# Kernel tuning notes

Measured on AMD Instinct MI355X. Metric: run time of the kernel, lower is better.

Reference implementation:

```python
import jax, jax.numpy as jnp
import numpy as np

IN_F = 1024
OUT_F = 1024
B, S = 8, 4096


def _pack_ternary(tern):
    # encoding: -1 -> 0, 0 -> 1, +1 -> 2; 4 values per byte, matching torch pack_ternary_weights
    enc = (tern + 1.0).astype(jnp.int32).reshape(-1)  # length divisible by 4 here
    return (enc[0::4] | (enc[1::4] << 2) | (enc[2::4] << 4) | (enc[3::4] << 6)).astype(jnp.int32)


def setup_inputs() -> dict:
    key = jax.random.key(0)
    kx, kw = jax.random.split(key)
    x = jax.random.normal(kx, (B, S, IN_F), dtype=jnp.float32)
    w = jax.random.normal(kw, (OUT_F, IN_F), dtype=jnp.float32) * 0.02
    # quantize_weights_158bit
    scale = jnp.maximum(jnp.mean(jnp.abs(w)), 1e-5)
    wn = w / scale
    tern = jnp.sign(wn) * (jnp.abs(wn) > 0.5).astype(jnp.float32)
    packed = _pack_ternary(tern)
    bias = jnp.zeros((OUT_F,), dtype=jnp.float32)
    return {"x": x, "packed_weight": packed, "weight_scale": scale.reshape(1), "bias": bias}


def reference(x, packed_weight, weight_scale, bias):
    n = OUT_F * IN_F
    shifts = jnp.array([0, 2, 4, 6], dtype=jnp.int32)
    # Faithful to original unpack_ternary_weights: concatenate bit-planes, then truncate.
    # (This is a permutation of the packed order, replicated deliberately.)
    enc = ((packed_weight[None, :] >> shifts[:, None]) & 3).reshape(-1)[:n]
    w = (enc.astype(jnp.float32) - 1.0).reshape(OUT_F, IN_F) * weight_scale  # dequant ternary
    # training path: INT8 per-token activation fake-quant
    act_scale = 127.0 / jnp.maximum(jnp.max(jnp.abs(x), axis=-1, keepdims=True), 1e-5)
    x_dq = jnp.clip(jnp.round(x * act_scale), -128.0, 127.0) / act_scale
    return jnp.einsum('bsi,oi->bso', x_dq, w) + bias
```

## Files before the change

### kernel.cpp

```cpp
#include <hip/hip_runtime.h>
#include <hip/hip_bf16.h>
#include <stdint.h>

typedef int i32x4 __attribute__((ext_vector_type(4)));

constexpr int IN_F = 1024;
constexpr int OUT_F = 1024;
constexpr int M_TOT = 8 * 4096;
constexpr int K_TOT = IN_F;
constexpr int N_TOT = OUT_F;

__global__ __launch_bounds__(256) void quant_kernel(
    const float* __restrict__ x,
    const float* __restrict__ wscale,
    int8_t* __restrict__ q,
    float* __restrict__ inv_row)
{
    const int row = blockIdx.x;
    const int t = threadIdx.x;
    const float4 v = reinterpret_cast<const float4*>(x + (size_t)row * IN_F)[t];
    float m = fmaxf(fmaxf(fabsf(v.x), fabsf(v.y)), fmaxf(fabsf(v.z), fabsf(v.w)));
    #pragma unroll
    for (int off = 32; off > 0; off >>= 1)
        m = fmaxf(m, __shfl_xor(m, off));
    __shared__ float smax[4];
    if ((t & 63) == 0) smax[t >> 6] = m;
    __syncthreads();
    m = fmaxf(fmaxf(smax[0], smax[1]), fmaxf(smax[2], smax[3]));
    const float a = fmaxf(m, 1e-5f);
    const float as = 127.0f / a;

    char4 o;
    o.x = (char)(int)fminf(fmaxf(rintf(v.x * as), -128.0f), 127.0f);
    o.y = (char)(int)fminf(fmaxf(rintf(v.y * as), -128.0f), 127.0f);
    o.z = (char)(int)fminf(fmaxf(rintf(v.z * as), -128.0f), 127.0f);
    o.w = (char)(int)fminf(fmaxf(rintf(v.w * as), -128.0f), 127.0f);
    reinterpret_cast<char4*>(q + (size_t)row * IN_F)[t] = o;
    if (t == 0) inv_row[row] = (a / 127.0f) * wscale[0];
}

__global__ __launch_bounds__(256) void unpack_kernel(
    const int* __restrict__ packed,
    int8_t* __restrict__ wt)
{
    const int o = blockIdx.x;
    const int k0 = threadIdx.x * 4;
    const int sh = (o >> 8) * 2;
    const int pbase = ((o & 255) << 10) + k0;
    const int4 pw = *reinterpret_cast<const int4*>(packed + pbase);
    char4 r;
    r.x = (char)(((pw.x >> sh) & 3) - 1);
    r.y = (char)(((pw.y >> sh) & 3) - 1);
    r.z = (char)(((pw.z >> sh) & 3) - 1);
    r.w = (char)(((pw.w >> sh) & 3) - 1);
    *reinterpret_cast<char4*>(wt + (size_t)o * IN_F + k0) = r;
}

constexpr int BM = 256, BN = 256, BK = 128;
constexpr int NT = K_TOT / BK;

__global__ __launch_bounds__(512, 2) void gemm_kernel(
    const int8_t* __restrict__ qa,
    const int8_t* __restrict__ wb,
    const float* __restrict__ inv_row,
    const float* __restrict__ bias,
    float* __restrict__ out)
{
    int bid = blockIdx.x;
    bid = (bid & 7) * ((int)gridDim.x >> 3) + (bid >> 3);
    const int tm = bid >> 2;
    const int tn = bid & 3;

    const int tid = threadIdx.x;
    const int lane = tid & 63;
    const int wid = tid >> 6;
    const int wr = wid >> 2;
    const int wc = wid & 3;

    __shared__ int8_t lds[2][2][2][128 * 128];

    const int rowA0 = tm * BM;
    const int rowB0 = tn * BN;
    const int frow = lane & 15;
    const int fq = lane >> 4;

    i32x4 acc[8][4] = {};

    auto stage = [&](int buf, int ab, int region, int kt) {
        const int8_t* base = ab ? wb : qa;
        #pragma unroll
        for (int j = 0; j < 2; ++j) {
            const int c = j * 512 + tid;
            const int rl = c >> 3, cc = c & 7;
            const int grow = ab ? (rowB0 + region * 128 + rl)
                                : (rowA0 + (rl & 64) * 2 + region * 64 + (rl & 63));
            const int scc = cc ^ (rl & 7);
            const int8_t* src = base + (size_t)grow * K_TOT + kt * BK + scc * 16;
            __builtin_amdgcn_global_load_lds(
                (const __attribute__((address_space(1))) void*)src,
                (__attribute__((address_space(3))) void*)&lds[buf][ab][region][c * 16],
                16, 0, 0);
        }
    };

    auto ldA = [&](int buf, int region, int mf, int ks) -> i32x4 {
        const int local = wr * 64 + (mf & 3) * 16 + frow;
        const int ch = (ks * 4 + fq) ^ (local & 7);
        return *reinterpret_cast<const i32x4*>(&lds[buf][0][region][local * 128 + ch * 16]);
    };
    auto ldB = [&](int buf, int nf, int ks) -> i32x4 {
        const int region = wc >> 1;
        const int local = (wc & 1) * 64 + nf * 16 + frow;
        const int ch = (ks * 4 + fq) ^ (local & 7);
        return *reinterpret_cast<const i32x4*>(&lds[buf][1][region][local * 128 + ch * 16]);
    };

    stage(0, 1, 0, 0); stage(0, 1, 1, 0); stage(0, 0, 0, 0); stage(0, 0, 1, 0);
    asm volatile("s_waitcnt vmcnt(0)" ::: "memory");
    __builtin_amdgcn_s_barrier();

    for (int T = 0; T < NT; ++T) {
        const int cur = T & 1, nxt = cur ^ 1;
        const bool st = (T + 1 < NT);
        i32x4 aF[4][2], bF[4][2];

        #pragma unroll
        for (int mf = 0; mf < 4; ++mf)
            #pragma unroll
            for (int ks = 0; ks < 2; ++ks)
                aF[mf][ks] = ldA(cur, 0, mf, ks);
        #pragma unroll
        for (int nf = 0; nf < 4; ++nf)
            #pragma unroll
            for (int ks = 0; ks < 2; ++ks)
                bF[nf][ks] = ldB(cur, nf, ks);
        if (st) { stage(nxt, 1, 0, T + 1); stage(nxt, 1, 1, T + 1); }
        __builtin_amdgcn_s_barrier();
        asm volatile("s_waitcnt lgkmcnt(0)" ::: "memory");
        __builtin_amdgcn_sched_barrier(0);
        __builtin_amdgcn_s_setprio(1);
        #pragma unroll
        for (int mf = 0; mf < 4; ++mf)
            #pragma unroll
            for (int nf = 0; nf < 4; ++nf)
                #pragma unroll
                for (int ks = 0; ks < 2; ++ks)
                    acc[mf][nf] = __builtin_amdgcn_mfma_i32_16x16x64_i8(
                        aF[mf][ks], bF[nf][ks], acc[mf][nf], 0, 0, 0);
        __builtin_amdgcn_s_setprio(0);
        if (st) asm volatile("s_waitcnt vmcnt(4)" ::: "memory");
        else    asm volatile("s_waitcnt vmcnt(0)" ::: "memory");
        __builtin_amdgcn_s_barrier();

        #pragma unroll
        for (int mf = 0; mf < 4; ++mf)
            #pragma unroll
            for (int ks = 0; ks < 2; ++ks)
                aF[mf][ks] = ldA(cur, 1, mf, ks);
        if (st) { stage(nxt, 0, 0, T + 1); stage(nxt, 0, 1, T + 1); }
        __builtin_amdgcn_s_barrier();
        asm volatile("s_waitcnt lgkmcnt(0)" ::: "memory");
        __builtin_amdgcn_sched_barrier(0);
        __builtin_amdgcn_s_setprio(1);
        #pragma unroll
        for (int mf = 0; mf < 4; ++mf)
            #pragma unroll
            for (int nf = 0; nf < 4; ++nf)
                #pragma unroll
                for (int ks = 0; ks < 2; ++ks)
                    acc[4 + mf][nf] = __builtin_amdgcn_mfma_i32_16x16x64_i8(
                        aF[mf][ks], bF[nf][ks], acc[4 + mf][nf], 0, 0, 0);
        __builtin_amdgcn_s_setprio(0);
        asm volatile("s_waitcnt vmcnt(2)" ::: "memory");
        __builtin_amdgcn_s_barrier();
    }

    #pragma unroll
    for (int mi = 0; mi < 8; ++mi) {
        #pragma unroll
        for (int j = 0; j < 4; ++j) {
            const int gm = rowA0 + wr * 128 + mi * 16 + fq * 4 + j;
            const float sc = inv_row[gm];
            #pragma unroll
            for (int nf = 0; nf < 4; ++nf) {
                const int gn = rowB0 + wc * 64 + nf * 16 + frow;
                out[(size_t)gm * N_TOT + gn] = (float)acc[mi][nf][j] * sc + bias[gn];
            }
        }
    }
}

extern "C" void kernel_launch(void* const* d_in, const int* in_sizes, int n_in,
                              void* d_out, int out_size, void* d_ws, size_t ws_size,
                              hipStream_t stream) {
    const float* x = (const float*)d_in[0];
    const int* packed = (const int*)d_in[1];
    const float* wscale = (const float*)d_in[2];
    const float* bias = (const float*)d_in[3];
    float* out = (float*)d_out;

    int8_t* q = (int8_t*)d_ws;
    int8_t* wt = (int8_t*)((char*)d_ws + (size_t)M_TOT * K_TOT);
    float* inv_row = (float*)((char*)d_ws + (size_t)M_TOT * K_TOT + (size_t)N_TOT * K_TOT);

    quant_kernel<<<M_TOT, 256, 0, stream>>>(x, wscale, q, inv_row);
    unpack_kernel<<<OUT_F, 256, 0, stream>>>(packed, wt);
    gemm_kernel<<<(M_TOT / BM) * (N_TOT / BN), 512, 0, stream>>>(q, wt, inv_row, bias, out);
}
```

Before: 86.79 us.

## Shrink GEMM tile to 256x128 with three-region LDS pipeline and split phases

New measurement: 88.48 us. No clear change (+2.0%).

```diff
diff --git a/kernel.cpp b/kernel.cpp
--- a/kernel.cpp
+++ b/kernel.cpp
@@ -56,7 +56,7 @@
     *reinterpret_cast<char4*>(wt + (size_t)o * IN_F + k0) = r;
 }
 
-constexpr int BM = 256, BN = 256, BK = 128;
+constexpr int BM = 256, BN = 128, BK = 128;
 constexpr int NT = K_TOT / BK;
 
 __global__ __launch_bounds__(512, 2) void gemm_kernel(
@@ -68,122 +68,158 @@
 {
     int bid = blockIdx.x;
     bid = (bid & 7) * ((int)gridDim.x >> 3) + (bid >> 3);
-    const int tm = bid >> 2;
-    const int tn = bid & 3;
+    const int tm = bid >> 3;
+    const int tn = bid & 7;
 
     const int tid = threadIdx.x;
     const int lane = tid & 63;
     const int wid = tid >> 6;
-    const int wr = wid >> 2;
-    const int wc = wid & 3;
-
-    __shared__ int8_t lds[2][2][2][128 * 128];
+    const int wr = wid >> 1;
+    const int wc = wid & 1;
+
+    __shared__ int8_t lds[2][3][128 * 128];
 
     const int rowA0 = tm * BM;
     const int rowB0 = tn * BN;
     const int frow = lane & 15;
     const int fq = lane >> 4;
 
-    i32x4 acc[8][4] = {};
-
-    auto stage = [&](int buf, int ab, int region, int kt) {
-        const int8_t* base = ab ? wb : qa;
+    i32x4 acc[4][4] = {};
+
+    auto stage = [&](int buf, int reg, int kt) {
         #pragma unroll
         for (int j = 0; j < 2; ++j) {
             const int c = j * 512 + tid;
             const int rl = c >> 3, cc = c & 7;
-            const int grow = ab ? (rowB0 + region * 128 + rl)
-                                : (rowA0 + (rl & 64) * 2 + region * 64 + (rl & 63));
             const int scc = cc ^ (rl & 7);
-            const int8_t* src = base + (size_t)grow * K_TOT + kt * BK + scc * 16;
+            const int8_t* src;
+            if (reg == 2)
+                src = wb + (size_t)(rowB0 + rl) * K_TOT + kt * BK + scc * 16;
+            else
+                src = qa + (size_t)(rowA0 + (rl >> 5) * 64 + reg * 32 + (rl & 31)) * K_TOT
+                         + kt * BK + scc * 16;
             __builtin_amdgcn_global_load_lds(
                 (const __attribute__((address_space(1))) void*)src,
-                (__attribute__((address_space(3))) void*)&lds[buf][ab][region][c * 16],
+                (__attribute__((address_space(3))) void*)&lds[buf][reg][c * 16],
                 16, 0, 0);
         }
     };
 
-    auto ldA = [&](int buf, int region, int mf, int ks) -> i32x4 {
-        const int local = wr * 64 + (mf & 3) * 16 + frow;
+    auto ldA = [&](int buf, int mf, int ks) -> i32x4 {
+        const int local = wr * 32 + (mf & 1) * 16 + frow;
         const int ch = (ks * 4 + fq) ^ (local & 7);
-        return *reinterpret_cast<const i32x4*>(&lds[buf][0][region][local * 128 + ch * 16]);
+        return *reinterpret_cast<const i32x4*>(&lds[buf][mf >> 1][local * 128 + ch * 16]);
     };
     auto ldB = [&](int buf, int nf, int ks) -> i32x4 {
-        const int region = wc >> 1;
-        const int local = (wc & 1) * 64 + nf * 16 + frow;
+        const int local = wc * 64 + (nf >> 1) * 32 + (nf & 1) * 16 + frow;
         const int ch = (ks * 4 + fq) ^ (local & 7);
-        return *reinterpret_cast<const i32x4*>(&lds[buf][1][region][local * 128 + ch * 16]);
+        return *reinterpret_cast<const i32x4*>(&lds[buf][2][local * 128 + ch * 16]);
     };
 
-    stage(0, 1, 0, 0); stage(0, 1, 1, 0); stage(0, 0, 0, 0); stage(0, 0, 1, 0);
+    stage(0, 2, 0); stage(0, 0, 0); stage(0, 1, 0);
     asm volatile("s_waitcnt vmcnt(0)" ::: "memory");
     __builtin_amdgcn_s_barrier();
 
     for (int T = 0; T < NT; ++T) {
         const int cur = T & 1, nxt = cur ^ 1;
         const bool st = (T + 1 < NT);
-        i32x4 aF[4][2], bF[4][2];
-
-        #pragma unroll
-        for (int mf = 0; mf < 4; ++mf)
-            #pragma unroll
-            for (int ks = 0; ks < 2; ++ks)
-                aF[mf][ks] = ldA(cur, 0, mf, ks);
-        #pragma unroll
-        for (int nf = 0; nf < 4; ++nf)
-            #pragma unroll
-            for (int ks = 0; ks < 2; ++ks)
-                bF[nf][ks] = ldB(cur, nf, ks);
-        if (st) { stage(nxt, 1, 0, T + 1); stage(nxt, 1, 1, T + 1); }
+        i32x4 aF[2][2], bF0[2][2], bF1[2][2];
+
+        #pragma unroll
+        for (int mf = 0; mf < 2; ++mf)
+            #pragma unroll
+            for (int ks = 0; ks < 2; ++ks)
+                aF[mf][ks] = ldA(cur, mf, ks);
+        #pragma unroll
+        for (int nf = 0; nf < 2; ++nf)
+            #pragma unroll
+            for (int ks = 0; ks < 2; ++ks)
+                bF0[nf][ks] = ldB(cur, nf, ks);
+        if (st) stage(nxt, 2, T + 1);
         __builtin_amdgcn_s_barrier();
         asm volatile("s_waitcnt lgkmcnt(0)" ::: "memory");
         __builtin_amdgcn_sched_barrier(0);
         __builtin_amdgcn_s_setprio(1);
         #pragma unroll
-        for (int mf = 0; mf < 4; ++mf)
-            #pragma unroll
-            for (int nf = 0; nf < 4; ++nf)
+        for (int mf = 0; mf < 2; ++mf)
+            #pragma unroll
+            for (int nf = 0; nf < 2; ++nf)
                 #pragma unroll
                 for (int ks = 0; ks < 2; ++ks)
                     acc[mf][nf] = __builtin_amdgcn_mfma_i32_16x16x64_i8(
-                        aF[mf][ks], bF[nf][ks], acc[mf][nf], 0, 0, 0);
+                        aF[mf][ks], bF0[nf][ks], acc[mf][nf], 0, 0, 0);
+        __builtin_amdgcn_s_setprio(0);
+        __builtin_amdgcn_s_barrier();
+
+        #pragma unroll
+        for (int nf = 0; nf < 2; ++nf)
+            #pragma unroll
+            for (int ks = 0; ks < 2; ++ks)
+                bF1[nf][ks] = ldB(cur, 2 + nf, ks);
+        if (st) stage(nxt, 0, T + 1);
+        __builtin_amdgcn_s_barrier();
+        asm volatile("s_waitcnt lgkmcnt(0)" ::: "memory");
+        __builtin_amdgcn_sched_barrier(0);
+        __builtin_amdgcn_s_setprio(1);
+        #pragma unroll
+        for (int mf = 0; mf < 2; ++mf)
+            #pragma unroll
+            for (int nf = 0; nf < 2; ++nf)
+                #pragma unroll
+                for (int ks = 0; ks < 2; ++ks)
+                    acc[mf][2 + nf] = __builtin_amdgcn_mfma_i32_16x16x64_i8(
+                        aF[mf][ks], bF1[nf][ks], acc[mf][2 + nf], 0, 0, 0);
         __builtin_amdgcn_s_setprio(0);
         if (st) asm volatile("s_waitcnt vmcnt(4)" ::: "memory");
         else    asm volatile("s_waitcnt vmcnt(0)" ::: "memory");
         __builtin_amdgcn_s_barrier();
 
         #pragma unroll
-        for (int mf = 0; mf < 4; ++mf)
-            #pragma unroll
-            for (int ks = 0; ks < 2; ++ks)
-                aF[mf][ks] = ldA(cur, 1, mf, ks);
-        if (st) { stage(nxt, 0, 0, T + 1); stage(nxt, 0, 1, T + 1); }
+        for (int mf = 0; mf < 2; ++mf)
+            #pragma unroll
+            for (int ks = 0; ks < 2; ++ks)
+                aF[mf][ks] = ldA(cur, 2 + mf, ks);
+        if (st) stage(nxt, 1, T + 1);
         __builtin_amdgcn_s_barrier();
         asm volatile("s_waitcnt lgkmcnt(0)" ::: "memory");
         __builtin_amdgcn_sched_barrier(0);
         __builtin_amdgcn_s_setprio(1);
         #pragma unroll
-        for (int mf = 0; mf < 4; ++mf)
-            #pragma unroll
-            for (int nf = 0; nf < 4; ++nf)
-                #pragma unroll
-                for (int ks = 0; ks < 2; ++ks)
-                    acc[4 + mf][nf] = __builtin_amdgcn_mfma_i32_16x16x64_i8(
-                        aF[mf][ks], bF[nf][ks], acc[4 + mf][nf], 0, 0, 0);
-        __builtin_amdgcn_s_setprio(0);
-        asm volatile("s_waitcnt vmcnt(2)" ::: "memory");
-        __builtin_amdgcn_s_barrier();
+        for (int mf = 0; mf < 2; ++mf)
+            #pragma unroll
+            for (int nf = 0; nf < 2; ++nf)
+                #pragma unroll
+                for (int ks = 0; ks < 2; ++ks)
+                    acc[2 + mf][2 + nf] = __builtin_amdgcn_mfma_i32_16x16x64_i8(
+                        aF[mf][ks], bF1[nf][ks], acc[2 + mf][2 + nf], 0, 0, 0);
+        __builtin_amdgcn_s_setprio(0);
+        __builtin_amdgcn_s_barrier();
+
+        __builtin_amdgcn_s_setprio(1);
+        #pragma unroll
+        for (int mf = 0; mf < 2; ++mf)
+            #pragma unroll
+            for (int nf = 0; nf < 2; ++nf)
+                #pragma unroll
+                for (int ks = 0; ks < 2; ++ks)
+                    acc[2 + mf][nf] = __builtin_amdgcn_mfma_i32_16x16x64_i8(
+                        aF[mf][ks], bF0[nf][ks], acc[2 + mf][nf], 0, 0, 0);
+        __builtin_amdgcn_s_setprio(0);
+        if (st) {
+            asm volatile("s_waitcnt vmcnt(2)" ::: "memory");
+            __builtin_amdgcn_s_barrier();
+        }
     }
 
     #pragma unroll
-    for (int mi = 0; mi < 8; ++mi) {
+    for (int mi = 0; mi < 4; ++mi) {
         #pragma unroll
         for (int j = 0; j < 4; ++j) {
-            const int gm = rowA0 + wr * 128 + mi * 16 + fq * 4 + j;
+            const int gm = rowA0 + wr * 64 + mi * 16 + fq * 4 + j;
             const float sc = inv_row[gm];
             #pragma unroll
             for (int nf = 0; nf < 4; ++nf) {
-                const int gn = rowB0 + wc * 64 + nf * 16 + frow;
+                const int gn = rowB0 + wc * 64 + (nf >> 1) * 32 + (nf & 1) * 16 + frow;
                 out[(size_t)gm * N_TOT + gn] = (float)acc[mi][nf][j] * sc + bias[gn];
             }
         }
```

## Triple-buffer A tiles and prefetch two k-steps ahead in int8 GEMM

Applied to the files above, without the earlier changes.

Result: slower. 90.94 us (+4.8%).

```diff
diff --git a/kernel.cpp b/kernel.cpp
--- a/kernel.cpp
+++ b/kernel.cpp
@@ -77,7 +77,8 @@
     const int wr = wid >> 2;
     const int wc = wid & 3;
 
-    __shared__ int8_t lds[2][2][2][128 * 128];
+    __shared__ int8_t ldsA[3][2][128 * 128];
+    __shared__ int8_t ldsB[2][2][128 * 128];
 
     const int rowA0 = tm * BM;
     const int rowB0 = tn * BN;
@@ -86,55 +87,69 @@
 
     i32x4 acc[8][4] = {};
 
-    auto stage = [&](int buf, int ab, int region, int kt) {
-        const int8_t* base = ab ? wb : qa;
+    auto stageA = [&](int slot, int region, int kt) {
         #pragma unroll
         for (int j = 0; j < 2; ++j) {
             const int c = j * 512 + tid;
             const int rl = c >> 3, cc = c & 7;
-            const int grow = ab ? (rowB0 + region * 128 + rl)
-                                : (rowA0 + (rl & 64) * 2 + region * 64 + (rl & 63));
             const int scc = cc ^ (rl & 7);
-            const int8_t* src = base + (size_t)grow * K_TOT + kt * BK + scc * 16;
+            const int8_t* src = qa + (size_t)(rowA0 + region * 128 + rl) * K_TOT
+                                   + kt * BK + scc * 16;
             __builtin_amdgcn_global_load_lds(
                 (const __attribute__((address_space(1))) void*)src,
-                (__attribute__((address_space(3))) void*)&lds[buf][ab][region][c * 16],
+                (__attribute__((address_space(3))) void*)&ldsA[slot][region][c * 16],
                 16, 0, 0);
         }
     };
-
-    auto ldA = [&](int buf, int region, int mf, int ks) -> i32x4 {
-        const int local = wr * 64 + (mf & 3) * 16 + frow;
+    auto stageB = [&](int slot, int region, int kt) {
+        #pragma unroll
+        for (int j = 0; j < 2; ++j) {
+            const int c = j * 512 + tid;
+            const int rl = c >> 3, cc = c & 7;
+            const int scc = cc ^ (rl & 7);
+            const int8_t* src = wb + (size_t)(rowB0 + region * 128 + rl) * K_TOT
+                                   + kt * BK + scc * 16;
+            __builtin_amdgcn_global_load_lds(
+                (const __attribute__((address_space(1))) void*)src,
+                (__attribute__((address_space(3))) void*)&ldsB[slot][region][c * 16],
+                16, 0, 0);
+        }
+    };
+
+    auto ldA = [&](int slot, int mf, int ks) -> i32x4 {
+        const int local = mf * 16 + frow;
         const int ch = (ks * 4 + fq) ^ (local & 7);
-        return *reinterpret_cast<const i32x4*>(&lds[buf][0][region][local * 128 + ch * 16]);
-    };
-    auto ldB = [&](int buf, int nf, int ks) -> i32x4 {
-        const int region = wc >> 1;
+        return *reinterpret_cast<const i32x4*>(&ldsA[slot][wr][(local * 8 + ch) * 16]);
+    };
+    auto ldB = [&](int slot, int nf, int ks) -> i32x4 {
         const int local = (wc & 1) * 64 + nf * 16 + frow;
         const int ch = (ks * 4 + fq) ^ (local & 7);
-        return *reinterpret_cast<const i32x4*>(&lds[buf][1][region][local * 128 + ch * 16]);
-    };
-
-    stage(0, 1, 0, 0); stage(0, 1, 1, 0); stage(0, 0, 0, 0); stage(0, 0, 1, 0);
-    asm volatile("s_waitcnt vmcnt(0)" ::: "memory");
-    __builtin_amdgcn_s_barrier();
+        return *reinterpret_cast<const i32x4*>(&ldsB[slot][wc >> 1][(local * 8 + ch) * 16]);
+    };
+
+    stageA(0, 0, 0); stageA(0, 1, 0);
+    stageB(0, 0, 0); stageB(0, 1, 0);
+    stageA(1, 0, 1); stageA(1, 1, 1);
 
     for (int T = 0; T < NT; ++T) {
-        const int cur = T & 1, nxt = cur ^ 1;
-        const bool st = (T + 1 < NT);
+        const int sa = T % 3, sb = T & 1;
+        if (T < NT - 1) asm volatile("s_waitcnt vmcnt(4)" ::: "memory");
+        else            asm volatile("s_waitcnt vmcnt(0)" ::: "memory");
+        __builtin_amdgcn_s_barrier();
+
         i32x4 aF[4][2], bF[4][2];
 
         #pragma unroll
-        for (int mf = 0; mf < 4; ++mf)
+        for (int nf = 0; nf < 4; ++nf)
             #pragma unroll
             for (int ks = 0; ks < 2; ++ks)
-                aF[mf][ks] = ldA(cur, 0, mf, ks);
-        #pragma unroll
-        for (int nf = 0; nf < 4; ++nf)
+                bF[nf][ks] = ldB(sb, nf, ks);
+        #pragma unroll
+        for (int mf = 0; mf < 4; ++mf)
             #pragma unroll
             for (int ks = 0; ks < 2; ++ks)
-                bF[nf][ks] = ldB(cur, nf, ks);
-        if (st) { stage(nxt, 1, 0, T + 1); stage(nxt, 1, 1, T + 1); }
+                aF[mf][ks] = ldA(sa, mf, ks);
+        if (T + 1 < NT) { stageB((T + 1) & 1, 0, T + 1); stageB((T + 1) & 1, 1, T + 1); }
         __builtin_amdgcn_s_barrier();
         asm volatile("s_waitcnt lgkmcnt(0)" ::: "memory");
         __builtin_amdgcn_sched_barrier(0);
@@ -148,16 +163,14 @@
                     acc[mf][nf] = __builtin_amdgcn_mfma_i32_16x16x64_i8(
                         aF[mf][ks], bF[nf][ks], acc[mf][nf], 0, 0, 0);
         __builtin_amdgcn_s_setprio(0);
-        if (st) asm volatile("s_waitcnt vmcnt(4)" ::: "memory");
-        else    asm volatile("s_waitcnt vmcnt(0)" ::: "memory");
         __builtin_amdgcn_s_barrier();
 
         #pragma unroll
         for (int mf = 0; mf < 4; ++mf)
             #pragma unroll
             for (int ks = 0; ks < 2; ++ks)
-                aF[mf][ks] = ldA(cur, 1, mf, ks);
-        if (st) { stage(nxt, 0, 0, T + 1); stage(nxt, 0, 1, T + 1); }
+                aF[mf][ks] = ldA(sa, 4 + mf, ks);
+        if (T + 2 < NT) { stageA((T + 2) % 3, 0, T + 2); stageA((T + 2) % 3, 1, T + 2); }
         __builtin_amdgcn_s_barrier();
         asm volatile("s_waitcnt lgkmcnt(0)" ::: "memory");
         __builtin_amdgcn_sched_barrier(0);
@@ -171,8 +184,6 @@
                     acc[4 + mf][nf] = __builtin_amdgcn_mfma_i32_16x16x64_i8(
                         aF[mf][ks], bF[nf][ks], acc[4 + mf][nf], 0, 0, 0);
         __builtin_amdgcn_s_setprio(0);
-        asm volatile("s_waitcnt vmcnt(2)" ::: "memory");
-        __builtin_amdgcn_s_barrier();
     }
 
     #pragma unroll
```

## Restructure int8 GEMM into smaller tiles with triple-buffered LDS pipeline

Applied to the files above, without the earlier changes.

New measurement: 89.57 us. 1.03x slower.

```diff
diff --git a/kernel.cpp b/kernel.cpp
--- a/kernel.cpp
+++ b/kernel.cpp
@@ -56,10 +56,10 @@
     *reinterpret_cast<char4*>(wt + (size_t)o * IN_F + k0) = r;
 }
 
-constexpr int BM = 256, BN = 256, BK = 128;
+constexpr int BM = 256, BN = 128, BK = 64;
 constexpr int NT = K_TOT / BK;
 
-__global__ __launch_bounds__(512, 2) void gemm_kernel(
+__global__ __launch_bounds__(512, 4) void gemm_kernel(
     const int8_t* __restrict__ qa,
     const int8_t* __restrict__ wb,
     const float* __restrict__ inv_row,
@@ -68,74 +68,74 @@
 {
     int bid = blockIdx.x;
     bid = (bid & 7) * ((int)gridDim.x >> 3) + (bid >> 3);
-    const int tm = bid >> 2;
-    const int tn = bid & 3;
+    const int tm = bid >> 3;
+    const int tn = bid & 7;
 
     const int tid = threadIdx.x;
     const int lane = tid & 63;
     const int wid = tid >> 6;
-    const int wr = wid >> 2;
-    const int wc = wid & 3;
+    const int wr = wid >> 1;
+    const int wc = wid & 1;
 
-    __shared__ int8_t lds[2][2][2][128 * 128];
+    __shared__ int8_t ldsA[3 * 256 * 64];
+    __shared__ int8_t ldsB[3 * 128 * 64];
 
     const int rowA0 = tm * BM;
     const int rowB0 = tn * BN;
     const int frow = lane & 15;
     const int fq = lane >> 4;
 
-    i32x4 acc[8][4] = {};
+    i32x4 acc[4][4] = {};
 
-    auto stage = [&](int buf, int ab, int region, int kt) {
-        const int8_t* base = ab ? wb : qa;
-        #pragma unroll
-        for (int j = 0; j < 2; ++j) {
-            const int c = j * 512 + tid;
-            const int rl = c >> 3, cc = c & 7;
-            const int grow = ab ? (rowB0 + region * 128 + rl)
-                                : (rowA0 + (rl & 64) * 2 + region * 64 + (rl & 63));
-            const int scc = cc ^ (rl & 7);
-            const int8_t* src = base + (size_t)grow * K_TOT + kt * BK + scc * 16;
-            __builtin_amdgcn_global_load_lds(
-                (const __attribute__((address_space(1))) void*)src,
-                (__attribute__((address_space(3))) void*)&lds[buf][ab][region][c * 16],
-                16, 0, 0);
-        }
+    const int r0 = tid >> 2;
+    const int scc0 = (tid & 3) ^ ((r0 >> 1) & 3);
+    const int8_t* srcA0 = qa + (size_t)(rowA0 + r0) * K_TOT + scc0 * 16;
+    const int8_t* srcB0 = wb + (size_t)(rowB0 + r0) * K_TOT + scc0 * 16;
+    const int dA0 = tid * 16, dA1 = (512 + tid) * 16;
+
+    auto stage = [&](int slot, int kt) {
+        __builtin_amdgcn_global_load_lds(
+            (const __attribute__((address_space(1))) void*)(srcA0 + kt * BK),
+            (__attribute__((address_space(3))) void*)&ldsA[slot * 16384 + dA0], 16, 0, 0);
+        __builtin_amdgcn_global_load_lds(
+            (const __attribute__((address_space(1))) void*)(srcA0 + (size_t)128 * K_TOT + kt * BK),
+            (__attribute__((address_space(3))) void*)&ldsA[slot * 16384 + dA1], 16, 0, 0);
+        __builtin_amdgcn_global_load_lds(
+            (const __attribute__((address_space(1))) void*)(srcB0 + kt * BK),
+            (__attribute__((address_space(3))) void*)&ldsB[slot * 8192 + dA0], 16, 0, 0);
     };
 
-    auto ldA = [&](int buf, int region, int mf, int ks) -> i32x4 {
-        const int local = wr * 64 + (mf & 3) * 16 + frow;
-        const int ch = (ks * 4 + fq) ^ (local & 7);
-        return *reinterpret_cast<const i32x4*>(&lds[buf][0][region][local * 128 + ch * 16]);
+    auto ldA = [&](int slot, int mf) -> i32x4 {
+        const int r = wr * 64 + mf * 16 + frow;
+        const int ch = fq ^ ((r >> 1) & 3);
+        return *reinterpret_cast<const i32x4*>(&ldsA[slot * 16384 + r * 64 + ch * 16]);
     };
-    auto ldB = [&](int buf, int nf, int ks) -> i32x4 {
-        const int region = wc >> 1;
-        const int local = (wc & 1) * 64 + nf * 16 + frow;
-        const int ch = (ks * 4 + fq) ^ (local & 7);
-        return *reinterpret_cast<const i32x4*>(&lds[buf][1][region][local * 128 + ch * 16]);
+    auto ldB = [&](int slot, int nf) -> i32x4 {
+        const int r = wc * 64 + nf * 16 + frow;
+        const int ch = fq ^ ((r >> 1) & 3);
+        return *reinterpret_cast<const i32x4*>(&ldsB[slot * 8192 + r * 64 + ch * 16]);
     };
 
-    stage(0, 1, 0, 0); stage(0, 1, 1, 0); stage(0, 0, 0, 0); stage(0, 0, 1, 0);
-    asm volatile("s_waitcnt vmcnt(0)" ::: "memory");
-    __builtin_amdgcn_s_barrier();
+    stage(0, 0);
+    stage(1, 1);
 
+    int sCur = 0;
     for (int T = 0; T < NT; ++T) {
-        const int cur = T & 1, nxt = cur ^ 1;
-        const bool st = (T + 1 < NT);
-        i32x4 aF[4][2], bF[4][2];
+        const int s = sCur;
+        const int s2 = (sCur + 2 >= 3) ? sCur - 1 : sCur + 2;
 
+        if (T < NT - 1) asm volatile("s_waitcnt vmcnt(3)" ::: "memory");
+        else            asm volatile("s_waitcnt vmcnt(0)" ::: "memory");
+        __builtin_amdgcn_s_barrier();
+
+        i32x4 aF[4], bF[4];
         #pragma unroll
-        for (int mf = 0; mf < 4; ++mf)
-            #pragma unroll
-            for (int ks = 0; ks < 2; ++ks)
-                aF[mf][ks] = ldA(cur, 0, mf, ks);
+        for (int mf = 0; mf < 4; ++mf) aF[mf] = ldA(s, mf);
         #pragma unroll
-        for (int nf = 0; nf < 4; ++nf)
-            #pragma unroll
-            for (int ks = 0; ks < 2; ++ks)
-                bF[nf][ks] = ldB(cur, nf, ks);
-        if (st) { stage(nxt, 1, 0, T + 1); stage(nxt, 1, 1, T + 1); }
-        __builtin_amdgcn_s_barrier();
+        for (int nf = 0; nf < 4; ++nf) bF[nf] = ldB(s, nf);
+
+        if (T + 2 < NT) stage(s2, T + 2);
+
         asm volatile("s_waitcnt lgkmcnt(0)" ::: "memory");
         __builtin_amdgcn_sched_barrier(0);
         __builtin_amdgcn_s_setprio(1);
@@ -143,48 +143,23 @@
         for (int mf = 0; mf < 4; ++mf)
             #pragma unroll
             for (int nf = 0; nf < 4; ++nf)
-                #pragma unroll
-                for (int ks = 0; ks < 2; ++ks)
-                    acc[mf][nf] = __builtin_amdgcn_mfma_i32_16x16x64_i8(
-                        aF[mf][ks], bF[nf][ks], acc[mf][nf], 0, 0, 0);
+                acc[mf][nf] = __builtin_amdgcn_mfma_i32_16x16x64_i8(
+                    aF[mf], bF[nf], acc[mf][nf], 0, 0, 0);
         __builtin_amdgcn_s_setprio(0);
-        if (st) asm volatile("s_waitcnt vmcnt(4)" ::: "memory");
-        else    asm volatile("s_waitcnt vmcnt(0)" ::: "memory");
-        __builtin_amdgcn_s_barrier();
 
-        #pragma unroll
-        for (int mf = 0; mf < 4; ++mf)
-            #pragma unroll
-            for (int ks = 0; ks < 2; ++ks)
-                aF[mf][ks] = ldA(cur, 1, mf, ks);
-        if (st) { stage(nxt, 0, 0, T + 1); stage(nxt, 0, 1, T + 1); }
-        __builtin_amdgcn_s_barrier();
-        asm volatile("s_waitcnt lgkmcnt(0)" ::: "memory");
-        __builtin_amdgcn_sched_barrier(0);
-        __builtin_amdgcn_s_setprio(1);
-        #pragma unroll
-        for (int mf = 0; mf < 4; ++mf)
-            #pragma unroll
-            for (int nf = 0; nf < 4; ++nf)
-                #pragma unroll
-                for (int ks = 0; ks < 2; ++ks)
-                    acc[4 + mf][nf] = __builtin_amdgcn_mfma_i32_16x16x64_i8(
-                        aF[mf][ks], bF[nf][ks], acc[4 + mf][nf], 0, 0, 0);
-        __builtin_amdgcn_s_setprio(0);
-        asm volatile("s_waitcnt vmcnt(2)" ::: "memory");
-        __builtin_amdgcn_s_barrier();
+        sCur = (sCur + 1 >= 3) ? 0 : sCur + 1;
     }
 
     #pragma unroll
-    for (int mi = 0; mi < 8; ++mi) {
+    for (int mf = 0; mf < 4; ++mf) {
         #pragma unroll
         for (int j = 0; j < 4; ++j) {
-            const int gm = rowA0 + wr * 128 + mi * 16 + fq * 4 + j;
+            const int gm = rowA0 + wr * 64 + mf * 16 + fq * 4 + j;
             const float sc = inv_row[gm];
             #pragma unroll
             for (int nf = 0; nf < 4; ++nf) {
                 const int gn = rowB0 + wc * 64 + nf * 16 + frow;
-                out[(size_t)gm * N_TOT + gn] = (float)acc[mi][nf][j] * sc + bias[gn];
+                out[(size_t)gm * N_TOT + gn] = (float)acc[mf][nf][j] * sc + bias[gn];
             }
         }
     }
```
